# Performance work log

Hardware: AMD Instinct MI355X
Metric: run time of the kernel (lower is better)

The kernel has to match this reference:

```python
import jax, jax.numpy as jnp
import numpy as np
import math

# batch, seq_len, emb_ch, convlru_hidden_ch, spatial H, W (W must equal H, see diag_embed broadcast)
B, L, E, C, H, W = 4, 32, 64, 96, 32, 32


def setup_inputs():
    key = jax.random.key(0)
    ks = jax.random.split(key, 24)
    r_min, r_max = 0.8, 0.99
    u1 = jax.random.uniform(ks[0], (C, H))
    u2 = jax.random.uniform(ks[1], (C, H))
    nu_log = jnp.log(-0.5 * jnp.log(u1 * (r_max ** 2 - r_min ** 2) + r_min ** 2))
    theta_log = jnp.log(u2 * 2.0 * np.pi)
    lam_abs = jnp.exp(-jnp.exp(nu_log))  # |lambda| = exp(-nu)
    gamma_log = jnp.log(jnp.sqrt(1.0 - lam_abs ** 2))
    params_log = jnp.vstack([nu_log, theta_log, gamma_log]).astype(jnp.float32)

    def w(k, shape, fan_in):
        s = 1.0 / np.sqrt(fan_in)
        return jax.random.uniform(k, shape, minval=-s, maxval=s, dtype=jnp.float32)

    return {
        "x": jax.random.normal(ks[2], (B, L, E, H, W), jnp.float32),
        "mask": jnp.ones((B, L), jnp.float32),
        "params_log": params_log,
        "Wb_r": w(ks[3], (C, E), E), "Wb_i": w(ks[4], (C, E), E),
        "bb_r": w(ks[5], (C,), E), "bb_i": w(ks[6], (C,), E),
        "Wp1_r": w(ks[7], (C, C), C), "Wp1_i": w(ks[8], (C, C), C),
        "bp1_r": w(ks[9], (C,), C), "bp1_i": w(ks[10], (C,), C),
        "Wp2_r": w(ks[11], (C, C), C), "Wp2_i": w(ks[12], (C, C), C),
        "bp2_r": w(ks[13], (C,), C), "bp2_i": w(ks[14], (C,), C),
        "Wc_r": w(ks[15], (E, C), C), "Wc_i": w(ks[16], (E, C), C),
        "bc_r": w(ks[17], (E,), C), "bc_i": w(ks[18], (E,), C),
        "ln_w": jnp.ones((E, H, W), jnp.float32),
        "ln_b": jnp.zeros((E, H, W), jnp.float32),
    }


def _forward(x, mask, params_log, Wb, bb, Wp1, bp1, Wp2, bp2, Wc, bc, ln_w, ln_b):
    nu, theta, gamma = jnp.split(jnp.exp(params_log), 3, axis=0)  # each (C, H)
    lamb = jnp.exp(jnp.complex64(-nu + 1j * theta))               # (C, H)
    xc = x.astype(jnp.complex64)
    # proj_B: 1x1 complex conv == channel einsum
    h = jnp.einsum('blehw,ce->blchw', xc, Wb) + bb[:, None, None]
    h = jnp.fft.fft2(h)  # over last two axes
    h = jnp.einsum('blkhw,ck->blchw', h, Wp1) + bp1[:, None, None]
    eye = jnp.eye(H, dtype=jnp.float32)  # (H, W); requires W == H
    # h * torch.diag_embed(gamma): elementwise mult with a diagonal (C,H,H) matrix
    # -> zeroes off-diagonal spatial entries (faithful to the torch code)
    h = h * (gamma[:, :, None] * eye)
    m = jnp.broadcast_to(mask[:, :, None, None, None], h.shape).astype(jnp.float32)
    log2L = int(math.ceil(math.log2(L)))
    lamb = lamb[None]  # (1, C, H)
    for i in range(1, log2L + 1):
        l = 2 ** i
        if i > 1:
            lamb = jnp.concatenate([lamb, lamb * lamb[-1]], axis=0)  # (l//2, C, H)
        hr = h.reshape(B * L // l, l, C, H, W)
        mr = m.reshape(B * L // l, l, C, H, W)
        h1, h2 = hr[:, : l // 2], hr[:, l // 2:]
        # term[n,j,c,a,b] = lamb[j,c,a] * eye[a,b] * h1[n,-1,c,a,b] * mask[n,l//2-1,c,a,b]
        term = (lamb[None, :, :, :, None] * eye) * h1[:, -1:] * mr[:, l // 2 - 1: l // 2]
        h = jnp.concatenate([h1, h2 + term], axis=1).reshape(B, L, C, H, W)
    h = jnp.fft.ifft2(h)
    h = jnp.einsum('blkhw,ck->blchw', h, Wp2) + bp2[:, None, None]
    h = jnp.einsum('blchw,ec->blehw', h, Wc) + bc[:, None, None]
    h = h.real
    # dropout is identity in eval mode
    mu = jnp.mean(h, axis=(-3, -2, -1), keepdims=True)
    var = jnp.var(h, axis=(-3, -2, -1), keepdims=True)
    h = (h - mu) / jnp.sqrt(var + 1e-5) * ln_w + ln_b
    return h + x


def reference(x, mask, params_log, Wb_r, Wb_i, bb_r, bb_i, Wp1_r, Wp1_i, bp1_r, bp1_i, Wp2_r, Wp2_i, bp2_r, bp2_i, Wc_r, Wc_i, bc_r, bc_i, ln_w, ln_b):
    cx = lambda r, i: (r + 1j * i).astype(jnp.complex64)
    return _forward(x, mask, params_log,
                    cx(Wb_r, Wb_i), cx(bb_r, bb_i),
                    cx(Wp1_r, Wp1_i), cx(bp1_r, bp1_i),
                    cx(Wp2_r, Wp2_i), cx(bp2_r, bp2_i),
                    cx(Wc_r, Wc_i), cx(bc_r, bc_i),
                    ln_w, ln_b)
```

## Files before the change

kernel.cpp:

```cpp
#include <hip/hip_runtime.h>

static constexpr int BL = 128;
static constexpr int OFF_COS  = 0;
static constexpr int OFF_SIN  = 1024;
static constexpr int OFF_ARE  = 2048;
static constexpr int OFF_AIM  = 8192;
static constexpr int OFF_WRE  = 14336;
static constexpr int OFF_WIM  = 20480;
static constexpr int OFF_LRE  = 26624;
static constexpr int OFF_LIM  = 29696;
static constexpr int OFF_GAM  = 32768;
static constexpr int OFF_BH0R = 35840;
static constexpr int OFF_BH0I = 35936;
static constexpr int OFF_BRR  = 36032;
static constexpr int OFF_QF   = 36096;
static constexpr int OFF_Y    = 560384;
static constexpr int OFF_V    = 1346816;
static constexpr int OFF_R    = 1871104;
static constexpr int OFF_ST   = 2133248;

__global__ __launch_bounds__(256) void k0_precompute(
    const float* __restrict__ params_log,
    const float* __restrict__ Wb_r, const float* __restrict__ Wb_i,
    const float* __restrict__ bb_r, const float* __restrict__ bb_i,
    const float* __restrict__ Wp1_r, const float* __restrict__ Wp1_i,
    const float* __restrict__ Wp2_r, const float* __restrict__ Wp2_i,
    const float* __restrict__ Wc_r, const float* __restrict__ Wc_i,
    const float* __restrict__ bp2_r, const float* __restrict__ bp2_i,
    const float* __restrict__ bc_r, float* __restrict__ ws) {
  int tid = blockIdx.x * 256 + threadIdx.x;
  if (tid < 1024) {
    int h = tid >> 5, s = tid & 31;
    int m = (h * s) & 31;
    float ang = (float)m * 0.19634954084936207f;
    ws[OFF_COS + tid] = cosf(ang);
    ws[OFF_SIN + tid] = sinf(ang);
  } else if (tid < 4096) {
    int i = tid - 1024;
    float nu = expf(params_log[i]);
    float th = expf(params_log[3072 + i]);
    float g  = expf(params_log[6144 + i]);
    float rr = expf(-nu);
    ws[OFF_LRE + i] = rr * cosf(th);
    ws[OFF_LIM + i] = rr * sinf(th);
    ws[OFF_GAM + i] = g;
  } else if (tid < 10240) {
    int i = tid - 4096;
    int c = i >> 6, e = i & 63;
    float are = 0.f, aim = 0.f;
    for (int k = 0; k < 96; ++k) {
      float pr = Wp1_r[c * 96 + k], pi = Wp1_i[c * 96 + k];
      float wr = Wb_r[k * 64 + e], wi = Wb_i[k * 64 + e];
      are += pr * wr - pi * wi;
      aim += pr * wi + pi * wr;
    }
    ws[OFF_ARE + i] = are;
    ws[OFF_AIM + i] = aim;
  } else if (tid < 16384) {
    int i = tid - 10240;
    int e = i / 96, c = i - e * 96;
    float are = 0.f, aim = 0.f;
    for (int k = 0; k < 96; ++k) {
      float wr = Wc_r[e * 96 + k], wi = Wc_i[e * 96 + k];
      float pr = Wp2_r[k * 96 + c], pi = Wp2_i[k * 96 + c];
      are += wr * pr - wi * pi;
      aim += wr * pi + wi * pr;
    }
    ws[OFF_WRE + i] = are;
    ws[OFF_WIM + i] = aim;
  } else if (tid < 16480) {
    int c = tid - 16384;
    float re = 0.f, im = 0.f;
    for (int k = 0; k < 96; ++k) {
      float pr = Wp1_r[c * 96 + k], pi = Wp1_i[c * 96 + k];
      float br = bb_r[k], bi = bb_i[k];
      re += pr * br - pi * bi;
      im += pr * bi + pi * br;
    }
    ws[OFF_BH0R + c] = 1024.f * re;
    ws[OFF_BH0I + c] = 1024.f * im;
  } else if (tid < 16544) {
    int e = tid - 16480;
    float re = 0.f;
    for (int k = 0; k < 96; ++k)
      re += Wc_r[e * 96 + k] * bp2_r[k] - Wc_i[e * 96 + k] * bp2_i[k];
    ws[OFF_BRR + e] = re + bc_r[e];
  }
}

__global__ __launch_bounds__(256) void k1_qdft(const float* __restrict__ x,
                                               float* __restrict__ ws) {
  __shared__ float pl[4][1024];
  __shared__ float qsh[4][32];
  int wave = threadIdx.x >> 6, lane = threadIdx.x & 63;
  int plane = blockIdx.x * 4 + wave;
  const float* xp = x + (size_t)plane * 1024;
#pragma unroll
  for (int j = 0; j < 16; ++j) pl[wave][j * 64 + lane] = xp[j * 64 + lane];
  __syncthreads();
  int s = lane & 31, half = lane >> 5;
  float acc = 0.f;
#pragma unroll
  for (int u0 = 0; u0 < 16; ++u0) {
    int u = half * 16 + u0;
    acc += pl[wave][u * 32 + ((s - u) & 31)];
  }
  acc += __shfl_xor(acc, 32);
  if (lane < 32) qsh[wave][lane] = acc;
  __syncthreads();
  int h = lane & 31;
  const float* Ft = ws + (lane < 32 ? OFF_COS : OFF_SIN);
  float sum = 0.f;
#pragma unroll
  for (int s2 = 0; s2 < 32; ++s2) sum += qsh[wave][s2] * Ft[s2 * 32 + h];
  if (lane >= 32) sum = -sum;
  ws[OFF_QF + plane * 64 + h * 2 + (lane < 32 ? 0 : 1)] = sum;
}

__global__ __launch_bounds__(256) void k2_mix1(float* __restrict__ ws,
                                               const float* __restrict__ bp1_r,
                                               const float* __restrict__ bp1_i) {
  __shared__ float qre[64][32], qim[64][32];
  int bl = blockIdx.x / 12, chunk = blockIdx.x % 12;
  const float2* qF = (const float2*)(ws + OFF_QF) + bl * 2048;
  for (int i = threadIdx.x; i < 2048; i += 256) {
    float2 v = qF[i];
    qre[i >> 5][i & 31] = v.x;
    qim[i >> 5][i & 31] = v.y;
  }
  __syncthreads();
  int c = chunk * 8 + (threadIdx.x >> 5), h = threadIdx.x & 31;
  const float* Ar = ws + OFF_ARE + c * 64;
  const float* Ai = ws + OFF_AIM + c * 64;
  float re = 0.f, im = 0.f;
#pragma unroll 8
  for (int e = 0; e < 64; ++e) {
    float ar = Ar[e], ai = Ai[e], qr = qre[e][h], qi = qim[e][h];
    re += ar * qr - ai * qi;
    im += ar * qi + ai * qr;
  }
  if (h == 0) { re += ws[OFF_BH0R + c]; im += ws[OFF_BH0I + c]; }
  re += bp1_r[c];
  im += bp1_i[c];
  float g = ws[OFF_GAM + c * 32 + h];
  ((float2*)(ws + OFF_Y))[(bl * 96 + c) * 32 + h] = make_float2(g * re, g * im);
}

__global__ __launch_bounds__(256) void k3_scan(float* __restrict__ ws,
                                               const float* __restrict__ mask) {
  int tid = blockIdx.x * 256 + threadIdx.x;
  int b = tid / 3072, r = tid - b * 3072;
  float lr = ws[OFF_LRE + r], li = ws[OFF_LIM + r];
  float2* Y = (float2*)(ws + OFF_Y) + (size_t)b * 32 * 3072 + r;
  float2 v = Y[0];
  float sr = v.x, si = v.y;
  for (int l = 1; l < 32; ++l) {
    float m = mask[b * 32 + l - 1];
    float cr = m * (lr * sr - li * si);
    float ci = m * (lr * si + li * sr);
    v = Y[l * 3072];
    sr = v.x + cr;
    si = v.y + ci;
    Y[l * 3072] = make_float2(sr, si);
  }
}

__global__ __launch_bounds__(256) void k4_mix2(float* __restrict__ ws) {
  __shared__ float sre[96][32], sim_[96][32];
  int bl = blockIdx.x >> 3, chunk = blockIdx.x & 7;
  const float2* S = (const float2*)(ws + OFF_Y) + bl * 3072;
  for (int i = threadIdx.x; i < 3072; i += 256) {
    float2 v = S[i];
    sre[i >> 5][i & 31] = v.x;
    sim_[i >> 5][i & 31] = v.y;
  }
  __syncthreads();
  int e = chunk * 8 + (threadIdx.x >> 5), h = threadIdx.x & 31;
  const float* Wr = ws + OFF_WRE + e * 96;
  const float* Wi = ws + OFF_WIM + e * 96;
  float re = 0.f, im = 0.f;
#pragma unroll 8
  for (int c = 0; c < 96; ++c) {
    float wr = Wr[c], wi = Wi[c], a = sre[c][h], b2 = sim_[c][h];
    re += wr * a - wi * b2;
    im += wr * b2 + wi * a;
  }
  ((float2*)(ws + OFF_V))[(bl * 64 + e) * 32 + h] = make_float2(re, im);
}

__global__ __launch_bounds__(256) void k5a_post(float* __restrict__ ws) {
  __shared__ float vre[64][32], vim[64][32];
  __shared__ float red[8];
  int bl = blockIdx.x;
  const float2* V = (const float2*)(ws + OFF_V) + bl * 2048;
  for (int i = threadIdx.x; i < 2048; i += 256) {
    float2 v = V[i];
    vre[i >> 5][i & 31] = v.x;
    vim[i >> 5][i & 31] = v.y;
  }
  __syncthreads();
  float sum = 0.f, sumsq = 0.f;
  float* R = ws + OFF_R + bl * 2048;
  for (int i = threadIdx.x; i < 2048; i += 256) {
    int e = i >> 5, s = i & 31;
    float acc = 0.f;
#pragma unroll
    for (int h = 0; h < 32; ++h)
      acc += vre[e][h] * ws[OFF_COS + h * 32 + s] - vim[e][h] * ws[OFF_SIN + h * 32 + s];
    float r = acc * (1.0f / 1024.0f) + ws[OFF_BRR + e];
    R[i] = r;
    sum += r;
    sumsq += r * r;
  }
#pragma unroll
  for (int off = 32; off > 0; off >>= 1) {
    sum += __shfl_down(sum, off);
    sumsq += __shfl_down(sumsq, off);
  }
  int wave = threadIdx.x >> 6, lane = threadIdx.x & 63;
  if (lane == 0) { red[wave] = sum; red[4 + wave] = sumsq; }
  __syncthreads();
  if (threadIdx.x == 0) {
    float s0 = red[0] + red[1] + red[2] + red[3];
    float q0 = red[4] + red[5] + red[6] + red[7];
    float mu = s0 * (1.0f / 2048.0f);
    float var = q0 * (1.0f / 2048.0f) - mu * mu;
    ws[OFF_ST + bl * 2] = mu;
    ws[OFF_ST + bl * 2 + 1] = rsqrtf(var + 1e-5f);
  }
}

__global__ __launch_bounds__(256) void k5b_final(const float* __restrict__ x,
                                                 const float* __restrict__ lnw,
                                                 const float* __restrict__ lnb,
                                                 const float* __restrict__ ws,
                                                 float* __restrict__ out) {
  int gid = blockIdx.x * 256 + threadIdx.x;
  int flat = gid * 4;
  int bl = flat >> 16;
  int rem = flat & 65535;
  int e = rem >> 10;
  int pos = rem & 1023;
  int u = pos >> 5, v = pos & 31;
  float mu = ws[OFF_ST + bl * 2], istd = ws[OFF_ST + bl * 2 + 1];
  const float* Rrow = ws + OFF_R + bl * 2048 + e * 32;
  const float4 xin = ((const float4*)x)[gid];
  const float4 lw = ((const float4*)lnw)[rem >> 2];
  const float4 lb = ((const float4*)lnb)[rem >> 2];
  float4 o;
  o.x = (Rrow[(u + v) & 31] - mu) * istd * lw.x + lb.x + xin.x;
  o.y = (Rrow[(u + v + 1) & 31] - mu) * istd * lw.y + lb.y + xin.y;
  o.z = (Rrow[(u + v + 2) & 31] - mu) * istd * lw.z + lb.z + xin.z;
  o.w = (Rrow[(u + v + 3) & 31] - mu) * istd * lw.w + lb.w + xin.w;
  ((float4*)out)[gid] = o;
}

extern "C" void kernel_launch(void* const* d_in, const int* in_sizes, int n_in,
                              void* d_out, int out_size, void* d_ws, size_t ws_size,
                              hipStream_t stream) {
  const float* x          = (const float*)d_in[0];
  const float* mask       = (const float*)d_in[1];
  const float* params_log = (const float*)d_in[2];
  const float* Wb_r  = (const float*)d_in[3];
  const float* Wb_i  = (const float*)d_in[4];
  const float* bb_r  = (const float*)d_in[5];
  const float* bb_i  = (const float*)d_in[6];
  const float* Wp1_r = (const float*)d_in[7];
  const float* Wp1_i = (const float*)d_in[8];
  const float* bp1_r = (const float*)d_in[9];
  const float* bp1_i = (const float*)d_in[10];
  const float* Wp2_r = (const float*)d_in[11];
  const float* Wp2_i = (const float*)d_in[12];
  const float* bp2_r = (const float*)d_in[13];
  const float* bp2_i = (const float*)d_in[14];
  const float* Wc_r  = (const float*)d_in[15];
  const float* Wc_i  = (const float*)d_in[16];
  const float* bc_r  = (const float*)d_in[17];
  const float* ln_w  = (const float*)d_in[19];
  const float* ln_b  = (const float*)d_in[20];
  float* ws  = (float*)d_ws;
  float* out = (float*)d_out;

  k0_precompute<<<65, 256, 0, stream>>>(params_log, Wb_r, Wb_i, bb_r, bb_i,
                                        Wp1_r, Wp1_i, Wp2_r, Wp2_i, Wc_r, Wc_i,
                                        bp2_r, bp2_i, bc_r, ws);
  k1_qdft<<<2048, 256, 0, stream>>>(x, ws);
  k2_mix1<<<1536, 256, 0, stream>>>(ws, bp1_r, bp1_i);
  k3_scan<<<48, 256, 0, stream>>>(ws, mask);
  k4_mix2<<<1024, 256, 0, stream>>>(ws);
  k5a_post<<<128, 256, 0, stream>>>(ws);
  k5b_final<<<8192, 256, 0, stream>>>(x, ln_w, ln_b, ws, out);
}
```

Before: 174.3 us.

## Fuse channel mix with post DFT, batch scan loads, vectorize plane loads

The second channel-mixing kernel and the post-processing inverse DFT kernel become one kernel per (b,l), so the intermediate V tensor stays in shared memory and never goes through global memory. Cos/sin tables are staged into LDS. The scan kernel now loads all 32 timesteps and mask values into registers before the recurrence, and the qdft kernel uses float4 loads. The fused kernel launches only 128 blocks with heavier LDS use, where the old mix kernel had 1024 blocks, so parallelism drops.

```diff
diff --git a/kernel.cpp b/kernel.cpp
--- a/kernel.cpp
+++ b/kernel.cpp
@@ -15,7 +15,6 @@
 static constexpr int OFF_BRR  = 36032;
 static constexpr int OFF_QF   = 36096;
 static constexpr int OFF_Y    = 560384;
-static constexpr int OFF_V    = 1346816;
 static constexpr int OFF_R    = 1871104;
 static constexpr int OFF_ST   = 2133248;
 
@@ -94,9 +93,10 @@
   __shared__ float qsh[4][32];
   int wave = threadIdx.x >> 6, lane = threadIdx.x & 63;
   int plane = blockIdx.x * 4 + wave;
-  const float* xp = x + (size_t)plane * 1024;
-#pragma unroll
-  for (int j = 0; j < 16; ++j) pl[wave][j * 64 + lane] = xp[j * 64 + lane];
+  const float4* xp4 = (const float4*)(x + (size_t)plane * 1024);
+  float4* pl4 = (float4*)pl[wave];
+#pragma unroll
+  for (int j = 0; j < 4; ++j) pl4[j * 64 + lane] = xp4[j * 64 + lane];
   __syncthreads();
   int s = lane & 31, half = lane >> 5;
   float acc = 0.f;
@@ -148,55 +148,61 @@
 
 __global__ __launch_bounds__(256) void k3_scan(float* __restrict__ ws,
                                                const float* __restrict__ mask) {
-  int tid = blockIdx.x * 256 + threadIdx.x;
-  int b = tid / 3072, r = tid - b * 3072;
+  int t = blockIdx.x * 256 + threadIdx.x;
+  int b = t / 3072, r = t - b * 3072;
   float lr = ws[OFF_LRE + r], li = ws[OFF_LIM + r];
   float2* Y = (float2*)(ws + OFF_Y) + (size_t)b * 32 * 3072 + r;
-  float2 v = Y[0];
-  float sr = v.x, si = v.y;
+  float2 v[32];
+#pragma unroll
+  for (int l = 0; l < 32; ++l) v[l] = Y[(size_t)l * 3072];
+  float m[31];
+#pragma unroll
+  for (int l = 0; l < 31; ++l) m[l] = mask[b * 32 + l];
+  float sr = v[0].x, si = v[0].y;
+#pragma unroll
   for (int l = 1; l < 32; ++l) {
-    float m = mask[b * 32 + l - 1];
-    float cr = m * (lr * sr - li * si);
-    float ci = m * (lr * si + li * sr);
-    v = Y[l * 3072];
-    sr = v.x + cr;
-    si = v.y + ci;
-    Y[l * 3072] = make_float2(sr, si);
-  }
-}
-
-__global__ __launch_bounds__(256) void k4_mix2(float* __restrict__ ws) {
+    float cr = m[l - 1] * (lr * sr - li * si);
+    float ci = m[l - 1] * (lr * si + li * sr);
+    sr = v[l].x + cr;
+    si = v[l].y + ci;
+    v[l] = make_float2(sr, si);
+  }
+#pragma unroll
+  for (int l = 1; l < 32; ++l) Y[(size_t)l * 3072] = v[l];
+}
+
+__global__ __launch_bounds__(256) void kB_mix2post(float* __restrict__ ws) {
   __shared__ float sre[96][32], sim_[96][32];
-  int bl = blockIdx.x >> 3, chunk = blockIdx.x & 7;
+  __shared__ float vre[64][32], vim[64][32];
+  __shared__ float tc[1024], tsn[1024];
+  __shared__ float red[8];
+  int bl = blockIdx.x;
   const float2* S = (const float2*)(ws + OFF_Y) + bl * 3072;
   for (int i = threadIdx.x; i < 3072; i += 256) {
     float2 v = S[i];
     sre[i >> 5][i & 31] = v.x;
     sim_[i >> 5][i & 31] = v.y;
   }
-  __syncthreads();
-  int e = chunk * 8 + (threadIdx.x >> 5), h = threadIdx.x & 31;
-  const float* Wr = ws + OFF_WRE + e * 96;
-  const float* Wi = ws + OFF_WIM + e * 96;
-  float re = 0.f, im = 0.f;
+  for (int i = threadIdx.x; i < 1024; i += 256) {
+    tc[i] = ws[OFF_COS + i];
+    tsn[i] = ws[OFF_SIN + i];
+  }
+  __syncthreads();
+  int h = threadIdx.x & 31;
+#pragma unroll
+  for (int rep = 0; rep < 8; ++rep) {
+    int e = rep * 8 + (threadIdx.x >> 5);
+    const float* Wr = ws + OFF_WRE + e * 96;
+    const float* Wi = ws + OFF_WIM + e * 96;
+    float re = 0.f, im = 0.f;
 #pragma unroll 8
-  for (int c = 0; c < 96; ++c) {
-    float wr = Wr[c], wi = Wi[c], a = sre[c][h], b2 = sim_[c][h];
-    re += wr * a - wi * b2;
-    im += wr * b2 + wi * a;
-  }
-  ((float2*)(ws + OFF_V))[(bl * 64 + e) * 32 + h] = make_float2(re, im);
-}
-
-__global__ __launch_bounds__(256) void k5a_post(float* __restrict__ ws) {
-  __shared__ float vre[64][32], vim[64][32];
-  __shared__ float red[8];
-  int bl = blockIdx.x;
-  const float2* V = (const float2*)(ws + OFF_V) + bl * 2048;
-  for (int i = threadIdx.x; i < 2048; i += 256) {
-    float2 v = V[i];
-    vre[i >> 5][i & 31] = v.x;
-    vim[i >> 5][i & 31] = v.y;
+    for (int c = 0; c < 96; ++c) {
+      float wr = Wr[c], wi = Wi[c], a = sre[c][h], b2 = sim_[c][h];
+      re += wr * a - wi * b2;
+      im += wr * b2 + wi * a;
+    }
+    vre[e][h] = re;
+    vim[e][h] = im;
   }
   __syncthreads();
   float sum = 0.f, sumsq = 0.f;
@@ -205,8 +211,8 @@
     int e = i >> 5, s = i & 31;
     float acc = 0.f;
 #pragma unroll
-    for (int h = 0; h < 32; ++h)
-      acc += vre[e][h] * ws[OFF_COS + h * 32 + s] - vim[e][h] * ws[OFF_SIN + h * 32 + s];
+    for (int h2 = 0; h2 < 32; ++h2)
+      acc += vre[e][h2] * tc[h2 * 32 + s] - vim[e][h2] * tsn[h2 * 32 + s];
     float r = acc * (1.0f / 1024.0f) + ws[OFF_BRR + e];
     R[i] = r;
     sum += r;
@@ -287,7 +293,6 @@
   k1_qdft<<<2048, 256, 0, stream>>>(x, ws);
   k2_mix1<<<1536, 256, 0, stream>>>(ws, bp1_r, bp1_i);
   k3_scan<<<48, 256, 0, stream>>>(ws, mask);
-  k4_mix2<<<1024, 256, 0, stream>>>(ws);
-  k5a_post<<<128, 256, 0, stream>>>(ws);
+  kB_mix2post<<<128, 256, 0, stream>>>(ws);
   k5b_final<<<8192, 256, 0, stream>>>(x, ln_w, ln_b, ws, out);
 }
```

New measurement: 185.7 us. 6.5% more time.
